# Kernel tuning notes

Hardware: AMD Instinct MI355X
Metric: run time of the kernel (lower is better)

Reference implementation:

```python
import jax, jax.numpy as jnp
import numpy as np

EPS = 1e-10


def setup_inputs() -> dict:
    key = jax.random.key(0)
    kx, ky = jax.random.split(key)
    x = jax.random.normal(kx, (8, 8192, 3), dtype=jnp.float32)
    y = jax.random.normal(ky, (8, 8192, 3), dtype=jnp.float32)
    return {"x": x, "y": y}


def reference(x, y):
    # x: (B, N, 3), y: (B, M, 3)
    xy = -2.0 * jnp.einsum("bnd,bmd->bnm", x, y)          # (B, N, M)
    xx = jnp.sum(x * x, axis=-1, keepdims=True)            # (B, N, 1)
    yy = jnp.sum(y * y, axis=-1, keepdims=True)            # (B, M, 1)
    dist = jnp.sqrt(xy + xx + jnp.swapaxes(yy, 1, 2) + EPS)  # (B, N, M)
    distance1 = jnp.min(dist, axis=2)                      # (B, N): x -> nearest y
    distance2 = jnp.min(dist, axis=1)                      # (B, M): y -> nearest x
    mean1 = jnp.mean(distance1, axis=-1)                   # (B,)
    mean2 = jnp.mean(distance2, axis=-1)                   # (B,)
    return jnp.sum(jnp.maximum(mean1, mean2))
```

## Files before the change

### kernel.cpp

```cpp
#include <hip/hip_runtime.h>


#define BB 8
#define NN 8192
#define NPTS (BB*NN)
#define BLK 256
#define CCOLS 256
#define CT 8
#define RT 4
#define STRIPS 16
#define GRID 512

typedef __attribute__((ext_vector_type(8))) short bf16x8;
typedef __attribute__((ext_vector_type(16))) float f32x16;

__device__ __forceinline__ unsigned f2mono(float f) {
    unsigned u = __float_as_uint(f);
    return u ^ ((unsigned)((int)u >> 31) | 0x80000000u);
}
__device__ __forceinline__ float mono2f(unsigned m) {
    unsigned u = ((int)m >= 0) ? ~m : (m ^ 0x80000000u);
    return __uint_as_float(u);
}
__device__ __forceinline__ unsigned bfh(float v) {
    unsigned u = __float_as_uint(v);
    u += 0x7FFFu + ((u >> 16) & 1u);
    return u >> 16;
}
__device__ __forceinline__ float bff(unsigned h) {
    return __uint_as_float(h << 16);
}
__device__ __forceinline__ unsigned pk(unsigned lo, unsigned hi) {
    return (lo & 0xFFFFu) | (hi << 16);
}

__global__ void prep_kernel(const float* __restrict__ x, const float* __restrict__ y,
                            uint4* __restrict__ afr, uint4* __restrict__ bfr,
                            unsigned* __restrict__ counter) {
    int i = blockIdx.x * BLK + threadIdx.x;
    if (i == 0) *counter = 0;
    const float* src = (i < NPTS) ? x : y;
    int j = (i < NPTS) ? i : i - NPTS;
    float c0 = src[3*j], c1 = src[3*j+1], c2 = src[3*j+2];
    float s2 = c0*c0 + c1*c1 + c2*c2;
    unsigned sh = bfh(s2), sl = bfh(s2 - bff(sh));
    float a0 = -2.f*c0, a1 = -2.f*c1, a2 = -2.f*c2;
    unsigned ah0 = bfh(a0), ah1 = bfh(a1), ah2 = bfh(a2);
    unsigned al0 = bfh(a0 - bff(ah0)), al1 = bfh(a1 - bff(ah1)), al2 = bfh(a2 - bff(ah2));
    unsigned bh0 = bfh(c0), bh1 = bfh(c1), bh2 = bfh(c2);
    unsigned bl0 = bfh(c0 - bff(bh0)), bl1 = bfh(c1 - bff(bh1)), bl2 = bfh(c2 - bff(bh2));
    const unsigned one = 0x3F80u;
    afr[2*i]   = make_uint4(pk(ah0,ah1), pk(ah2,al0), pk(al1,al2), pk(ah0,ah1));
    afr[2*i+1] = make_uint4(pk(ah2,sh),  pk(sl,one),  pk(one,0u),  0u);
    bfr[2*i]   = make_uint4(pk(bh0,bh1), pk(bh2,bh0), pk(bh1,bh2), pk(bl0,bl1));
    bfr[2*i+1] = make_uint4(pk(bl2,one), pk(one,sh),  pk(sl,0u),   0u);
}

__device__ __forceinline__ bf16x8 cvt(uint4 v) { return __builtin_bit_cast(bf16x8, v); }
__device__ __forceinline__ f32x16 vmin16(f32x16 a, f32x16 b) {
    f32x16 r;
#pragma unroll
    for (int i = 0; i < 16; ++i) r[i] = fminf(a[i], b[i]);
    return r;
}

__global__ __launch_bounds__(BLK, 2) void
main_kernel(const uint4* __restrict__ afr, const uint4* __restrict__ bfr,
            float* __restrict__ bpart, unsigned* __restrict__ counter,
            float* __restrict__ out) {
    __shared__ unsigned colmin[CCOLS];
    __shared__ float red[4];
    __shared__ float gg[16];
    __shared__ int lastflag;
    const int bi  = blockIdx.x;
    const int dir = bi >> 8;
    const int b   = (bi >> 5) & 7;
    const int cc  = bi & 31;
    const uint4* Af = afr + (dir ? 2*NPTS : 0);
    const uint4* Bf = bfr + (dir ? 0 : 2*NPTS);
    const int tid = threadIdx.x;
    const int lane = tid & 63, w = tid >> 6;
    const int m = lane & 31;
    const int hb = lane >> 5;

    colmin[tid] = 0xFFFFFFFFu;

    bf16x8 bf[CT];
#pragma unroll
    for (int ct = 0; ct < CT; ++ct) {
        int c = b * NN + cc * CCOLS + ct * 32 + m;
        bf[ct] = cvt(Bf[2*c + hb]);
    }

    f32x16 zro;
#pragma unroll
    for (int i = 0; i < 16; ++i) zro[i] = 0.f;

    f32x16 vm[CT];
#pragma unroll
    for (int ct = 0; ct < CT; ++ct) vm[ct] = zro + 3.4e38f;

    const int rowbase = b * NN + w * 128 + m;
    uint4 cur[RT], nxt[RT];
#pragma unroll
    for (int t = 0; t < RT; ++t) cur[t] = Af[2*(rowbase + t*32) + hb];

#pragma unroll 1
    for (int s = 0; s < STRIPS; ++s) {
        const int np = (s + 1 < STRIPS) ? (s + 1) : s;
#pragma unroll
        for (int t = 0; t < RT; ++t) nxt[t] = Af[2*(rowbase + np*512 + t*32) + hb];
#pragma unroll
        for (int t = 0; t < RT; ++t) {
            bf16x8 av = cvt(cur[t]);
#pragma unroll
            for (int ct = 0; ct < CT; ++ct) {
                f32x16 acc = __builtin_amdgcn_mfma_f32_32x32x16_bf16(av, bf[ct], zro, 0, 0, 0);
                vm[ct] = vmin16(vm[ct], acc);
            }
        }
#pragma unroll
        for (int t = 0; t < RT; ++t) cur[t] = nxt[t];
    }

#pragma unroll
    for (int ct = 0; ct < CT; ++ct) {
        f32x16 v = vm[ct];
        float p0 = fminf(fminf(v[0], v[1]), fminf(v[2], v[3]));
        float p1 = fminf(fminf(v[4], v[5]), fminf(v[6], v[7]));
        float p2 = fminf(fminf(v[8], v[9]), fminf(v[10], v[11]));
        float p3 = fminf(fminf(v[12], v[13]), fminf(v[14], v[15]));
        float p = fminf(fminf(p0, p1), fminf(p2, p3));
        p = fminf(p, __shfl_xor(p, 32, 64));
        if (hb == 0) atomicMin(&colmin[ct * 32 + m], f2mono(p));
    }
    __syncthreads();

    float d = sqrtf(fmaxf(mono2f(colmin[tid]), 0.f) + 1e-10f);
#pragma unroll
    for (int off = 32; off; off >>= 1) d += __shfl_down(d, off, 64);
    if (lane == 0) red[w] = d;
    __syncthreads();
    if (tid == 0) {
        float total = red[0] + red[1] + red[2] + red[3];
        atomicExch(&bpart[bi], total);
        __threadfence();
        unsigned old = atomicAdd(counter, 1u);
        lastflag = (old == GRID - 1);
    }
    __syncthreads();

    if (lastflag) {
        float v0 = atomicAdd(&bpart[tid], 0.f);
        float v1 = atomicAdd(&bpart[256 + tid], 0.f);
#pragma unroll
        for (int off = 16; off; off >>= 1) {
            v0 += __shfl_down(v0, off, 32);
            v1 += __shfl_down(v1, off, 32);
        }
        if ((tid & 31) == 0) gg[tid >> 5] = fmaxf(v0, v1);
        __syncthreads();
        if (tid == 0) {
            float acc = 0.f;
#pragma unroll
            for (int k = 0; k < 8; ++k) acc += gg[k];
            out[0] = acc * (1.0f / (float)NN);
        }
    }
}

extern "C" void kernel_launch(void* const* d_in, const int* in_sizes, int n_in,
                              void* d_out, int out_size, void* d_ws, size_t ws_size,
                              hipStream_t stream) {
    const float* x = (const float*)d_in[0];
    const float* y = (const float*)d_in[1];
    float* out = (float*)d_out;

    char* ws = (char*)d_ws;
    uint4* afr = (uint4*)ws;
    uint4* bfr = afr + 4 * NPTS;
    float* bpart = (float*)(bfr + 4 * NPTS);
    unsigned* counter = (unsigned*)(bpart + GRID);

    prep_kernel<<<(2 * NPTS) / BLK, BLK, 0, stream>>>(x, y, afr, bfr, counter);
    main_kernel<<<GRID, BLK, 0, stream>>>(afr, bfr, bpart, counter, out);
}
```

Before: 111.5 us.

## Halve column tile per block, double grid, and software-pipeline MFMA with min

```diff
diff --git a/kernel.cpp b/kernel.cpp
--- a/kernel.cpp
+++ b/kernel.cpp
@@ -5,11 +5,11 @@
 #define NN 8192
 #define NPTS (BB*NN)
 #define BLK 256
-#define CCOLS 256
-#define CT 8
+#define CCOLS 128
+#define CT 4
 #define RT 4
 #define STRIPS 16
-#define GRID 512
+#define GRID 1024
 
 typedef __attribute__((ext_vector_type(8))) short bf16x8;
 typedef __attribute__((ext_vector_type(16))) float f32x16;
@@ -73,9 +73,9 @@
     __shared__ float gg[16];
     __shared__ int lastflag;
     const int bi  = blockIdx.x;
-    const int dir = bi >> 8;
-    const int b   = (bi >> 5) & 7;
-    const int cc  = bi & 31;
+    const int dir = bi >> 9;
+    const int b   = (bi >> 6) & 7;
+    const int cc  = bi & 63;
     const uint4* Af = afr + (dir ? 2*NPTS : 0);
     const uint4* Bf = bfr + (dir ? 0 : 2*NPTS);
     const int tid = threadIdx.x;
@@ -83,7 +83,7 @@
     const int m = lane & 31;
     const int hb = lane >> 5;
 
-    colmin[tid] = 0xFFFFFFFFu;
+    if (tid < CCOLS) colmin[tid] = 0xFFFFFFFFu;
 
     bf16x8 bf[CT];
 #pragma unroll
@@ -110,15 +110,17 @@
         const int np = (s + 1 < STRIPS) ? (s + 1) : s;
 #pragma unroll
         for (int t = 0; t < RT; ++t) nxt[t] = Af[2*(rowbase + np*512 + t*32) + hb];
+
+        f32x16 accA = __builtin_amdgcn_mfma_f32_32x32x16_bf16(cvt(cur[0]), bf[0], zro, 0, 0, 0);
 #pragma unroll
-        for (int t = 0; t < RT; ++t) {
-            bf16x8 av = cvt(cur[t]);
-#pragma unroll
-            for (int ct = 0; ct < CT; ++ct) {
-                f32x16 acc = __builtin_amdgcn_mfma_f32_32x32x16_bf16(av, bf[ct], zro, 0, 0, 0);
-                vm[ct] = vmin16(vm[ct], acc);
-            }
+        for (int i = 0; i < RT * CT - 1; ++i) {
+            f32x16 accB = __builtin_amdgcn_mfma_f32_32x32x16_bf16(
+                cvt(cur[(i + 1) >> 2]), bf[(i + 1) & 3], zro, 0, 0, 0);
+            vm[i & 3] = vmin16(vm[i & 3], accA);
+            accA = accB;
         }
+        vm[3] = vmin16(vm[3], accA);
+
 #pragma unroll
         for (int t = 0; t < RT; ++t) cur[t] = nxt[t];
     }
@@ -136,7 +138,8 @@
     }
     __syncthreads();
 
-    float d = sqrtf(fmaxf(mono2f(colmin[tid]), 0.f) + 1e-10f);
+    float d = 0.f;
+    if (tid < CCOLS) d = sqrtf(fmaxf(mono2f(colmin[tid]), 0.f) + 1e-10f);
 #pragma unroll
     for (int off = 32; off; off >>= 1) d += __shfl_down(d, off, 64);
     if (lane == 0) red[w] = d;
@@ -151,19 +154,19 @@
     __syncthreads();
 
     if (lastflag) {
-        float v0 = atomicAdd(&bpart[tid], 0.f);
-        float v1 = atomicAdd(&bpart[256 + tid], 0.f);
+        const int g = tid >> 4, k = tid & 15;
+        float v = 0.f;
 #pragma unroll
-        for (int off = 16; off; off >>= 1) {
-            v0 += __shfl_down(v0, off, 32);
-            v1 += __shfl_down(v1, off, 32);
-        }
-        if ((tid & 31) == 0) gg[tid >> 5] = fmaxf(v0, v1);
+        for (int j = 0; j < 4; ++j)
+            v += atomicAdd(&bpart[g * 64 + k * 4 + j], 0.f);
+#pragma unroll
+        for (int off = 8; off; off >>= 1) v += __shfl_down(v, off, 16);
+        if (k == 0) gg[g] = v;
         __syncthreads();
         if (tid == 0) {
             float acc = 0.f;
 #pragma unroll
-            for (int k = 0; k < 8; ++k) acc += gg[k];
+            for (int bb = 0; bb < BB; ++bb) acc += fmaxf(gg[bb], gg[BB + bb]);
             out[0] = acc * (1.0f / (float)NN);
         }
     }
```

Measured after the change: 110.1 us. No clear change (-1.3%).
